# Kernel tuning notes

Hardware: AMD Instinct MI355X
Metric: run time of the kernel (lower is better)

Reference implementation:

```python
import jax, jax.numpy as jnp
import numpy as np
from jax import lax

B, C, H, W = 32, 3, 128, 128
D = 512   # embedding dim (= encoder channels)
K = 512   # codebook size
S = 4     # conv stride / kernel
HL = H // S  # 32
LL = HL * HL // 1  # latent spatial positions per image... (HL*WL)


def setup_inputs() -> dict:
    key = jax.random.key(0)
    k1, k2, k3, k4 = jax.random.split(key, 4)
    x = jax.random.uniform(k1, (B, C, H, W), dtype=jnp.float32)
    We = jax.random.normal(k2, (D, C, S, S), dtype=jnp.float32) * 0.05  # OIHW
    be = jnp.zeros((D,), dtype=jnp.float32)
    Wd = jax.random.normal(k3, (C, D, S, S), dtype=jnp.float32) * 0.05  # OIHW for conv_transpose
    bd = jnp.zeros((C,), dtype=jnp.float32)
    codebook = jax.random.normal(k4, (D, K), dtype=jnp.float32)  # NearestEmbed.weight: (emb_dim, n_emb)
    return {"x": x, "We": We, "be": be, "Wd": Wd, "bd": bd, "codebook": codebook}


def _encode(x, We, be):
    y = lax.conv_general_dilated(x, We, (S, S), 'VALID',
                                 dimension_numbers=('NCHW', 'OIHW', 'NCHW'))
    return jax.nn.relu(y + be[None, :, None, None])  # (B, D, HL, HL)


def _decode(z, Wd, bd):
    y = lax.conv_transpose(z, Wd, (S, S), 'VALID',
                           dimension_numbers=('NCHW', 'OIHW', 'NCHW'))
    return jax.nn.sigmoid(y + bd[None, :, None, None])  # (B, C, H, W)


def _nearest_idx(z, W):
    # z: (B, D, L), W: (D, K). Squared L2 distance via ||z||^2 - 2 z.W + ||W||^2.
    z2 = jnp.sum(z * z, axis=1)                 # (B, L)
    w2 = jnp.sum(W * W, axis=0)                 # (K,)
    cross = jnp.einsum('bdl,dk->blk', z, W)     # (B, L, K)
    dist = z2[:, :, None] - 2.0 * cross + w2[None, None, :]
    return jnp.argmin(dist, axis=-1)            # (B, L) int


def _gather(W, idx):
    # W: (D, K), idx: (B, L) -> (B, D, L)
    return jnp.take(W, idx, axis=1).transpose(1, 0, 2)


def reference(x, We, be, Wd, bd, codebook):
    code = _encode(x, We, be)                       # (B, D, HL, HL)
    z_e = code.reshape(code.shape[0], D, -1)        # (B, D, L)
    # 1) z_q with weight stop-grad + straight-through on input
    idx_q = _nearest_idx(z_e, codebook)
    zq_raw = _gather(lax.stop_gradient(codebook), idx_q)
    z_q = z_e + lax.stop_gradient(zq_raw - z_e)     # grad d z_q / d z_e = I
    # 2) emb with input detached (grad flows only to codebook via gather)
    ze_sg = lax.stop_gradient(z_e)
    idx_e = _nearest_idx(ze_sg, codebook)
    emb = _gather(codebook, idx_e)
    recon = _decode(z_q.reshape(code.shape), Wd, bd)
    return (recon, z_e.reshape(code.shape), emb.reshape(code.shape))
```

## Files before the change

kernel.cpp:

```cpp
#include <hip/hip_runtime.h>
#include <hip/hip_bf16.h>

#define NPOS 32768
#define EPS_GAP 4e-3f
#define MAXSUS 4096

typedef __attribute__((ext_vector_type(8))) short short8;
typedef __attribute__((ext_vector_type(4))) float floatx4;

static __device__ __forceinline__ float bfu(unsigned short h) {
    return __uint_as_float(((unsigned int)h) << 16);
}
static __device__ __forceinline__ unsigned short f2bf(float f) {
    unsigned int u = __float_as_uint(f);
    u = (u + 0x7fffu + ((u >> 16) & 1u)) >> 16;
    return (unsigned short)u;
}
static __device__ __forceinline__ float ldin(const void* p, size_t i, int flag) {
    return flag ? bfu(((const unsigned short*)p)[i]) : ((const float*)p)[i];
}

static __device__ __forceinline__ void ldsbar() {
    asm volatile("s_waitcnt lgkmcnt(0)" ::: "memory");
    __builtin_amdgcn_s_barrier();
    asm volatile("" ::: "memory");
}

static __device__ __forceinline__ size_t swzoff(int k, int d) {
    return (size_t)(d >> 5) * 16384 + (size_t)(k >> 4) * 512
         + (size_t)((((d >> 3) & 3) * 16 + (k & 15)) * 8) + (d & 7);
}

__global__ __launch_bounds__(256) void k_prepAll(
        const void* __restrict__ We, const void* __restrict__ be,
        const void* __restrict__ Wd, const void* __restrict__ bd,
        const void* __restrict__ cb,
        int* __restrict__ flagp, int* __restrict__ scnt,
        float* __restrict__ cbe,
        float* __restrict__ cbT, unsigned short* __restrict__ cbHS,
        unsigned short* __restrict__ cbLS,
        unsigned short* __restrict__ WeswzH, unsigned short* __restrict__ WeswzL,
        float* __restrict__ w2, double* __restrict__ w2d,
        float* __restrict__ U) {
    __shared__ float tile[64][65];
    __shared__ double sd[256];
    __shared__ float sf[256];
    __shared__ int sflag;
    const int bid = blockIdx.x;
    const int t = threadIdx.x;

    {
        const unsigned short* u = (const unsigned short*)cb;
        const int kc = t & 63, g = t >> 6;
        float a = 0.f;
        for (int d = g * 128; d < g * 128 + 128; ++d) {
            float v = bfu(u[(size_t)d * 512 + kc]);
            a = fmaf(v, v, a);
        }
        sf[t] = a;
        __syncthreads();
        if (t < 64) {
            float s = sf[t] + sf[t + 64] + sf[t + 128] + sf[t + 192];
            int ok = (s >= 100.f && s <= 2000.f) ? 1 : 0;
            unsigned long long m = __ballot(ok);
            if (t == 0) sflag = (m == ~0ull) ? 1 : 0;
        }
        __syncthreads();
    }
    const int flag = sflag;

    if (bid == 0) {
        if (t == 0) { *flagp = flag; *scnt = 0; }
        cbe[t]       = ldin(be, t, flag);
        cbe[t + 256] = ldin(be, t + 256, flag);
    } else if (bid < 65) {
        const int bb = bid - 1;
        const int D0 = (bb >> 3) * 64, K0 = (bb & 7) * 64;
        for (int it = 0; it < 16; ++it) {
            int r = (t >> 6) + 4 * it, c = t & 63;
            tile[r][c] = ldin(cb, (size_t)(D0 + r) * 512 + K0 + c, flag);
        }
        __syncthreads();
        for (int it = 0; it < 16; ++it) {
            int r = (t >> 6) + 4 * it, c = t & 63;
            float v = tile[c][r];
            int k = K0 + r, d = D0 + c;
            cbT[(size_t)k * 512 + d] = v;
            size_t o2 = swzoff(k, d);
            unsigned short h = f2bf(v);
            cbHS[o2] = h;
            cbLS[o2] = f2bf(v - bfu(h));
        }
    } else if (bid < 73) {
        const int k = (bid - 65) * 64 + (t & 63);
        const int g = t >> 6;
        double acc = 0.0;
        for (int d = g * 128; d < g * 128 + 128; ++d) {
            double v = (double)ldin(cb, (size_t)d * 512 + k, flag);
            acc += v * v;
        }
        sd[t] = acc;
        __syncthreads();
        if (t < 64) {
            double a = sd[t] + sd[t + 64] + sd[t + 128] + sd[t + 192];
            w2[k] = (float)a;
            w2d[k] = a;
        }
    } else if (bid < 201) {
        const int kk = (bid - 73) * 4 + (t >> 6);
        const int lane = t & 63;
        const int j = lane >> 2, dpart = lane & 3;
        const int u = (j >> 2) & 3, v = j & 3;
        int woff[3];
        #pragma unroll
        for (int m = 0; m < 3; ++m) woff[m] = m * 8192 + (3 - u) * 4 + (3 - v);
        float a0 = 0.f, a1 = 0.f, a2 = 0.f;
        for (int i = 0; i < 128; ++i) {
            int d = dpart * 128 + i;
            float cw = ldin(cb, (size_t)d * 512 + kk, flag);
            a0 = fmaf(cw, ldin(Wd, (size_t)(woff[0] + d * 16), flag), a0);
            a1 = fmaf(cw, ldin(Wd, (size_t)(woff[1] + d * 16), flag), a1);
            a2 = fmaf(cw, ldin(Wd, (size_t)(woff[2] + d * 16), flag), a2);
        }
        a0 += __shfl_xor(a0, 1); a0 += __shfl_xor(a0, 2);
        a1 += __shfl_xor(a1, 1); a1 += __shfl_xor(a1, 2);
        a2 += __shfl_xor(a2, 1); a2 += __shfl_xor(a2, 2);
        if (dpart == 0) {
            U[kk * 48 +  0 + j] = a0 + ldin(bd, 0, flag);
            U[kk * 48 + 16 + j] = a1 + ldin(bd, 1, flag);
            U[kk * 48 + 32 + j] = a2 + ldin(bd, 2, flag);
        }
    } else {
        const int bid2 = bid - 201;
        for (int it = 0; it < 16; ++it) {
            int e = bid2 * 4096 + it * 256 + t;
            int d = e >> 6, q = e & 63;
            float w = (q < 48) ? ldin(We, (size_t)d * 48 + q, flag) : 0.f;
            unsigned short h = f2bf(w);
            unsigned short l = f2bf(w - bfu(h));
            size_t off = (size_t)((d >> 5) * 2 + ((d >> 4) & 1)) * 1024
                       + (size_t)(q >> 5) * 512
                       + (size_t)((((q >> 3) & 3) * 16 + (d & 15)) * 8) + (q & 7);
            WeswzH[off] = h;
            WeswzL[off] = l;
        }
    }
}

static __device__ __forceinline__ void conv_mfma(
        const unsigned short* __restrict__ patchH, const unsigned short* __restrict__ patchL,
        const unsigned short* __restrict__ WeH, const unsigned short* __restrict__ WeL,
        const float* __restrict__ cbe, int dc, int wave, int lane, int flag,
        unsigned short* __restrict__ zq, float* __restrict__ out_z, int b, int SP0) {
    const int mt = wave >> 1, nt = wave & 1;
    const int quad = lane >> 4, lcol = lane & 15;
    const int row = mt * 16 + lcol;
    short8 aH0 = *(const short8*)(patchH + row * 72 + quad * 8);
    short8 aH1 = *(const short8*)(patchH + row * 72 + 32 + quad * 8);
    const unsigned short* wb = WeH + (size_t)((dc >> 5) * 2 + nt) * 1024 + lane * 8;
    short8 bH0 = *(const short8*)(wb);
    short8 bH1 = *(const short8*)(wb + 512);
    floatx4 c = (floatx4){0.f, 0.f, 0.f, 0.f};
    c = __builtin_amdgcn_mfma_f32_16x16x32_bf16(aH0, bH0, c, 0, 0, 0);
    c = __builtin_amdgcn_mfma_f32_16x16x32_bf16(aH1, bH1, c, 0, 0, 0);
    if (!flag) {
        short8 aL0 = *(const short8*)(patchL + row * 72 + quad * 8);
        short8 aL1 = *(const short8*)(patchL + row * 72 + 32 + quad * 8);
        const unsigned short* wl = WeL + (size_t)((dc >> 5) * 2 + nt) * 1024 + lane * 8;
        short8 bL0 = *(const short8*)(wl);
        short8 bL1 = *(const short8*)(wl + 512);
        c = __builtin_amdgcn_mfma_f32_16x16x32_bf16(aL0, bH0, c, 0, 0, 0);
        c = __builtin_amdgcn_mfma_f32_16x16x32_bf16(aL1, bH1, c, 0, 0, 0);
        c = __builtin_amdgcn_mfma_f32_16x16x32_bf16(aH0, bL0, c, 0, 0, 0);
        c = __builtin_amdgcn_mfma_f32_16x16x32_bf16(aH1, bL1, c, 0, 0, 0);
    }
    const int d = nt * 16 + lcol;
    const float bias = cbe[dc + d];
    const int p0 = mt * 16 + quad * 4;
    float zf[4];
    #pragma unroll
    for (int r = 0; r < 4; ++r) {
        float z = fmaxf(c[r] + bias, 0.f);
        unsigned short h = f2bf(z);
        unsigned short l = f2bf(z - bfu(h));
        zq[(p0 + r) * 40 + d] = h;
        zq[2560 + (p0 + r) * 40 + d] = l;
        zf[r] = bfu(h) + bfu(l);
    }
    *(float4*)(out_z + (size_t)(b * 512 + dc + d) * 1024 + SP0 + p0) =
        (float4){zf[0], zf[1], zf[2], zf[3]};
}

static __device__ __forceinline__ void mfma_step(
        const unsigned short* __restrict__ zq,
        const unsigned short* __restrict__ cbHS,
        const unsigned short* __restrict__ cbLS,
        int dcPrev, int wave, int quad, int lcol, int flag, floatx4 (&acc)[4][4]) {
    const int lane = quad * 16 + lcol;
    short8 aH[4], aL[4];
    #pragma unroll
    for (int mt = 0; mt < 4; ++mt) {
        aH[mt] = *(const short8*)(zq + (mt * 16 + lcol) * 40 + quad * 8);
        aL[mt] = *(const short8*)(zq + 2560 + (mt * 16 + lcol) * 40 + quad * 8);
    }
    const unsigned short* fbH = cbHS + (size_t)dcPrev * 512 + (size_t)(wave * 4) * 512 + lane * 8;
    #pragma unroll
    for (int j = 0; j < 4; ++j) {
        short8 bH = *(const short8*)(fbH + j * 512);
        #pragma unroll
        for (int mt = 0; mt < 4; ++mt) {
            acc[mt][j] = __builtin_amdgcn_mfma_f32_16x16x32_bf16(aH[mt], bH, acc[mt][j], 0, 0, 0);
            acc[mt][j] = __builtin_amdgcn_mfma_f32_16x16x32_bf16(aL[mt], bH, acc[mt][j], 0, 0, 0);
        }
    }
    if (!flag) {
        const unsigned short* fbL = cbLS + (size_t)dcPrev * 512 + (size_t)(wave * 4) * 512 + lane * 8;
        #pragma unroll
        for (int j = 0; j < 4; ++j) {
            short8 bL = *(const short8*)(fbL + j * 512);
            #pragma unroll
            for (int mt = 0; mt < 4; ++mt)
                acc[mt][j] = __builtin_amdgcn_mfma_f32_16x16x32_bf16(aH[mt], bL, acc[mt][j], 0, 0, 0);
        }
    }
}

static __device__ __forceinline__ void bmerge(float& a1, int& ak, float& a2,
                                              float o1, int ok, float o2) {
    if (o1 < a1)      { a2 = fminf(a1, o2); a1 = o1; ak = ok; }
    else if (o1 > a1) { a2 = fminf(a2, o1); }
    else              { a2 = a1; if (ok < ak) ak = ok; }
}

__global__ __launch_bounds__(512, 4) void k_main(
        const void* __restrict__ x, const unsigned short* __restrict__ WeswzH,
        const unsigned short* __restrict__ WeswzL,
        const float* __restrict__ cbe, const int* __restrict__ flagp,
        const unsigned short* __restrict__ cbHS, const unsigned short* __restrict__ cbLS,
        const float* __restrict__ cbT, const float* __restrict__ w2,
        float* __restrict__ out_z, float* __restrict__ out_e,
        int* __restrict__ idx, int* __restrict__ scnt, int* __restrict__ spos,
        int skipTail) {
    __shared__ __align__(16) char smc[38912];
    unsigned short* patchH = (unsigned short*)smc;
    unsigned short* patchL = (unsigned short*)(smc + 9216);
    unsigned short* zb = (unsigned short*)(smc + 18432);

    const int t = threadIdx.x;
    const int bid = blockIdx.x;
    const int q = ((bid & 7) << 6) | (bid >> 3);
    const int P0 = q * 64;
    const int b = P0 >> 10, SP0 = P0 & 1023;
    const int flag = *flagp;
    const int wave = t >> 6, lane = t & 63;
    const int quad = lane >> 4, lcol = lane & 15;

    for (int e = t; e < 4096; e += 512) {
        int pid = e >> 6, qq = e & 63;
        float xv = 0.f;
        if (qq < 48) {
            int c = qq >> 4, r = (qq >> 2) & 3, s = qq & 3;
            int pos = P0 + pid;
            int bb = pos >> 10, sp = pos & 1023, i = sp >> 5, j = sp & 31;
            xv = ldin(x, ((bb * 3 + c) * 128 + (i * 4 + r)) * 128 + (j * 4 + s), flag);
        }
        unsigned short h = f2bf(xv);
        patchH[pid * 72 + qq] = h;
        patchL[pid * 72 + qq] = f2bf(xv - bfu(h));
    }

    floatx4 acc[4][4];
    #pragma unroll
    for (int mt = 0; mt < 4; ++mt)
        #pragma unroll
        for (int j = 0; j < 4; ++j) acc[mt][j] = (floatx4){0.f, 0.f, 0.f, 0.f};

    ldsbar();
    conv_mfma(patchH, patchL, WeswzH, WeswzL, cbe, 0, wave, lane, flag,
              zb, out_z, b, SP0);
    for (int dc = 32; dc < 512; dc += 32) {
        ldsbar();
        const int p = (dc >> 5) & 1;
        conv_mfma(patchH, patchL, WeswzH, WeswzL, cbe, dc, wave, lane, flag,
                  zb + p * 5120, out_z, b, SP0);
        mfma_step(zb + (p ^ 1) * 5120, cbHS, cbLS, dc - 32, wave, quad, lcol, flag, acc);
    }
    ldsbar();
    mfma_step(zb + 5120, cbHS, cbLS, 480, wave, quad, lcol, flag, acc);

    float s1[4][4], s2[4][4]; int k1[4][4];
    #pragma unroll
    for (int mt = 0; mt < 4; ++mt)
        #pragma unroll
        for (int r = 0; r < 4; ++r) { s1[mt][r] = 1e30f; s2[mt][r] = 1e30f; k1[mt][r] = 511; }
    #pragma unroll
    for (int j = 0; j < 4; ++j) {
        int code = (wave * 4 + j) * 16 + lcol;
        float wk = w2[code];
        #pragma unroll
        for (int mt = 0; mt < 4; ++mt)
            #pragma unroll
            for (int r = 0; r < 4; ++r) {
                float s = wk - 2.f * acc[mt][j][r];
                bmerge(s1[mt][r], k1[mt][r], s2[mt][r], s, code, 1e30f);
            }
    }
    float* sS1 = (float*)smc;
    int*   sK1 = (int*)(smc + 2048);
    float* sS2 = (float*)(smc + 4096);
    int*   ii  = (int*)(smc + 6144);
    #pragma unroll
    for (int mt = 0; mt < 4; ++mt)
        #pragma unroll
        for (int r = 0; r < 4; ++r) {
            float a1 = s1[mt][r], a2 = s2[mt][r]; int ak = k1[mt][r];
            #pragma unroll
            for (int m = 1; m < 16; m <<= 1) {
                float o1 = __shfl_xor(a1, m);
                float o2 = __shfl_xor(a2, m);
                int   ok = __shfl_xor(ak, m);
                bmerge(a1, ak, a2, o1, ok, o2);
            }
            if (lcol == 0) {
                int pos = mt * 16 + quad * 4 + r;
                sS1[pos * 8 + wave] = a1;
                sK1[pos * 8 + wave] = ak;
                sS2[pos * 8 + wave] = a2;
            }
        }
    __syncthreads();
    if (t < 64) {
        float a1 = sS1[t * 8]; int ak = sK1[t * 8]; float a2 = sS2[t * 8];
        #pragma unroll
        for (int w = 1; w < 8; ++w)
            bmerge(a1, ak, a2, sS1[t * 8 + w], sK1[t * 8 + w], sS2[t * 8 + w]);
        ak &= 511;
        ii[t] = ak;
        unsigned int flagged = 0u;
        if (a2 - a1 < EPS_GAP) {
            int slot = atomicAdd(scnt, 1);
            if (slot < MAXSUS) { spos[slot] = P0 + t; flagged = 1u; }
        }
        idx[P0 + t] = (int)((unsigned)ak | (flagged << 31));
    }
    __syncthreads();

    const int sp = t & 63, dq = t >> 6;
    const float* row = cbT + (size_t)ii[sp] * 512;
    const size_t obase = ((size_t)b * 512) * 1024 + SP0 + sp;
    for (int d0 = dq * 64; d0 < dq * 64 + 64; d0 += 4) {
        if (skipTail && b == 31 && d0 >= 448) break;
        float4 v = *(const float4*)(row + d0);
        out_e[obase + (size_t)(d0    ) * 1024] = v.x;
        out_e[obase + (size_t)(d0 + 1) * 1024] = v.y;
        out_e[obase + (size_t)(d0 + 2) * 1024] = v.z;
        out_e[obase + (size_t)(d0 + 3) * 1024] = v.w;
    }
}

__global__ __launch_bounds__(256) void k_post(
        const float* __restrict__ out_z, const void* __restrict__ cb,
        const double* __restrict__ w2d, int* __restrict__ idx,
        const int* __restrict__ scnt, const int* __restrict__ spos,
        const float* __restrict__ U, const int* __restrict__ flagp,
        float* __restrict__ out_e, float* __restrict__ out_r, int skipTail) {
    __shared__ float zsh[512];
    __shared__ float rs[256];
    __shared__ int rk[256];
    __shared__ int bc[2];
    const int bid = blockIdx.x;
    const int t = threadIdx.x;

    if (bid < 128) {
        const int pos = bid * 256 + t;
        const int v0 = idx[pos];
        if (v0 >= 0) {
            const int id = v0 & 511;
            const int b = pos >> 10, sp = pos & 1023, i = sp >> 5, j = sp & 31;
            const float* u = &U[(size_t)id * 48];
            #pragma unroll
            for (int c = 0; c < 3; ++c)
                #pragma unroll
                for (int uu = 0; uu < 4; ++uu) {
                    float4 q = *(const float4*)(&u[c * 16 + uu * 4]);
                    float4 o;
                    o.x = 1.f / (1.f + __expf(-q.x));
                    o.y = 1.f / (1.f + __expf(-q.y));
                    o.z = 1.f / (1.f + __expf(-q.z));
                    o.w = 1.f / (1.f + __expf(-q.w));
                    *(float4*)(&out_r[((size_t)((b * 3 + c) * 128) + (i * 4 + uu)) * 128 + j * 4]) = o;
                }
        }
        return;
    }

    const int flag = *flagp;
    int n = *scnt; if (n > MAXSUS) n = MAXSUS;
    for (int s = bid - 128; s < n; s += 256) {
        int p = spos[s] & 32767;
        int b = p >> 10, sp = p & 1023;
        __syncthreads();
        zsh[t]       = out_z[(size_t)(b * 512 + t) * 1024 + sp];
        zsh[t + 256] = out_z[(size_t)(b * 512 + t + 256) * 1024 + sp];
        __syncthreads();
        float bs = 1e30f; int bk = 511;
        for (int cc = 0; cc < 2; ++cc) {
            int k = t + cc * 256;
            double a = 0.0;
            for (int d = 0; d < 512; ++d)
                a = fma((double)zsh[d], (double)ldin(cb, (size_t)d * 512 + k, flag), a);
            float sc = (float)(w2d[k] - 2.0 * a);
            if (sc < bs || (sc == bs && k < bk)) { bs = sc; bk = k; }
        }
        rs[t] = bs; rk[t] = bk;
        __syncthreads();
        for (int str = 128; str > 0; str >>= 1) {
            if (t < str) {
                float so = rs[t + str]; int ko = rk[t + str];
                if (so < rs[t] || (so == rs[t] && ko < rk[t])) { rs[t] = so; rk[t] = ko; }
            }
            __syncthreads();
        }
        if (t == 0) {
            int kstar = rk[0] & 511;
            int old = idx[p] & 511;
            bc[0] = kstar; bc[1] = (kstar != old);
            idx[p] = kstar;
        }
        __syncthreads();
        const int kk = bc[0];
        if (bc[1]) {
            for (int d = t; d < 512; d += 256) {
                if (skipTail && b == 31 && d >= 448) continue;
                out_e[(size_t)(b * 512 + d) * 1024 + sp] = ldin(cb, (size_t)d * 512 + kk, flag);
            }
        }
        if (t < 48) {
            float q = U[(size_t)kk * 48 + t];
            float o = 1.f / (1.f + __expf(-q));
            int c = t >> 4, uu = (t >> 2) & 3, vv = t & 3;
            int i = sp >> 5, j = sp & 31;
            out_r[((size_t)((b * 3 + c) * 128) + (i * 4 + uu)) * 128 + j * 4 + vv] = o;
        }
    }
}

__global__ __launch_bounds__(1024) void k_fixup(
        const void* __restrict__ cb, const int* __restrict__ flagp,
        const int* __restrict__ idx, float* __restrict__ out_e) {
    const int t = threadIdx.x;
    const int d = 448 + blockIdx.x;
    const int flag = *flagp;
    const int id = idx[31744 + t] & 511;
    out_e[((size_t)(31 * 512 + d)) * 1024 + t] = ldin(cb, (size_t)d * 512 + id, flag);
}

extern "C" void kernel_launch(void* const* d_in, const int* in_sizes, int n_in,
                              void* d_out, int out_size, void* d_ws, size_t ws_size,
                              hipStream_t stream) {
    const void* x  = d_in[0];
    const void* We = d_in[1];
    const void* be = d_in[2];
    const void* Wd = d_in[3];
    const void* bd = d_in[4];
    const void* cb = d_in[5];

    float* out   = (float*)d_out;
    float* out_r = out;
    float* out_z = out + 1572864;
    float* out_e = out + 18350080;

    char* Rb = (char*)out_r;
    float* cbT           = (float*)(Rb);
    float* cbe           = (float*)(Rb + 1146880);
    unsigned short* cbHS = (unsigned short*)(Rb + 1247296);
    unsigned short* cbLS = (unsigned short*)(Rb + 1771584);
    unsigned short* WeswzH=(unsigned short*)(Rb + 2295872);
    unsigned short* WeswzL=(unsigned short*)(Rb + 2361408);

    int tailWS = (ws_size >= 262144) ? 1 : 0;
    char* Tbase = tailWS ? (char*)d_ws : ((char*)out_e + 66846720);
    int skipTail = tailWS ? 0 : 1;
    int*    idx  = (int*)   (Tbase);
    float*  U    = (float*) (Tbase + 131072);
    float*  w2   = (float*) (Tbase + 229376);
    double* w2d  = (double*)(Tbase + 231424);
    int*    flag = (int*)   (Tbase + 235520);
    int*    scnt = (int*)   (Tbase + 235584);
    int*    spos = (int*)   (Tbase + 235648);

    k_prepAll<<<209, 256, 0, stream>>>(We, be, Wd, bd, cb, flag, scnt,
                                       cbe, cbT, cbHS, cbLS, WeswzH, WeswzL,
                                       w2, w2d, U);
    k_main<<<512, 512, 0, stream>>>(x, WeswzH, WeswzL, cbe, flag, cbHS, cbLS,
                                    cbT, w2, out_z, out_e, idx, scnt, spos,
                                    skipTail);
    k_post<<<384, 256, 0, stream>>>(out_z, cb, w2d, idx, scnt, spos, U, flag,
                                    out_e, out_r, skipTail);
    if (skipTail)
        k_fixup<<<64, 1024, 0, stream>>>(cb, flag, idx, out_e);
}
```

Baseline: 261.6 us.

## Move decoder-table computation into main kernel and double conv/MFMA pipeline stage depth

Precomputation of the per-code decoder table U moves out of the prep kernel into 64 extra blocks of the main kernel. The prep kernel shrinks and this work can overlap with the main encode/quantize blocks. The conv-to-codebook-MFMA pipeline now processes two 32-channel chunks per barrier using four LDS buffers instead of two, which halves the number of barriers. This raises static LDS from 38912 to 59392 bytes per block, which may lower occupancy under the 4-blocks-per-CU launch bound. The extra U blocks also compete with the main blocks for CUs.

```diff
diff --git a/kernel.cpp b/kernel.cpp
--- a/kernel.cpp
+++ b/kernel.cpp
@@ -33,15 +33,13 @@
 
 __global__ __launch_bounds__(256) void k_prepAll(
         const void* __restrict__ We, const void* __restrict__ be,
-        const void* __restrict__ Wd, const void* __restrict__ bd,
         const void* __restrict__ cb,
         int* __restrict__ flagp, int* __restrict__ scnt,
         float* __restrict__ cbe,
         float* __restrict__ cbT, unsigned short* __restrict__ cbHS,
         unsigned short* __restrict__ cbLS,
         unsigned short* __restrict__ WeswzH, unsigned short* __restrict__ WeswzL,
-        float* __restrict__ w2, double* __restrict__ w2d,
-        float* __restrict__ U) {
+        float* __restrict__ w2, double* __restrict__ w2d) {
     __shared__ float tile[64][65];
     __shared__ double sd[256];
     __shared__ float sf[256];
@@ -106,32 +104,8 @@
             w2[k] = (float)a;
             w2d[k] = a;
         }
-    } else if (bid < 201) {
-        const int kk = (bid - 73) * 4 + (t >> 6);
-        const int lane = t & 63;
-        const int j = lane >> 2, dpart = lane & 3;
-        const int u = (j >> 2) & 3, v = j & 3;
-        int woff[3];
-        #pragma unroll
-        for (int m = 0; m < 3; ++m) woff[m] = m * 8192 + (3 - u) * 4 + (3 - v);
-        float a0 = 0.f, a1 = 0.f, a2 = 0.f;
-        for (int i = 0; i < 128; ++i) {
-            int d = dpart * 128 + i;
-            float cw = ldin(cb, (size_t)d * 512 + kk, flag);
-            a0 = fmaf(cw, ldin(Wd, (size_t)(woff[0] + d * 16), flag), a0);
-            a1 = fmaf(cw, ldin(Wd, (size_t)(woff[1] + d * 16), flag), a1);
-            a2 = fmaf(cw, ldin(Wd, (size_t)(woff[2] + d * 16), flag), a2);
-        }
-        a0 += __shfl_xor(a0, 1); a0 += __shfl_xor(a0, 2);
-        a1 += __shfl_xor(a1, 1); a1 += __shfl_xor(a1, 2);
-        a2 += __shfl_xor(a2, 1); a2 += __shfl_xor(a2, 2);
-        if (dpart == 0) {
-            U[kk * 48 +  0 + j] = a0 + ldin(bd, 0, flag);
-            U[kk * 48 + 16 + j] = a1 + ldin(bd, 1, flag);
-            U[kk * 48 + 32 + j] = a2 + ldin(bd, 2, flag);
-        }
     } else {
-        const int bid2 = bid - 201;
+        const int bid2 = bid - 73;
         for (int it = 0; it < 16; ++it) {
             int e = bid2 * 4096 + it * 256 + t;
             int d = e >> 6, q = e & 63;
@@ -238,21 +212,50 @@
         const float* __restrict__ cbe, const int* __restrict__ flagp,
         const unsigned short* __restrict__ cbHS, const unsigned short* __restrict__ cbLS,
         const float* __restrict__ cbT, const float* __restrict__ w2,
+        const void* __restrict__ cb, const void* __restrict__ Wd,
+        const void* __restrict__ bd, float* __restrict__ U,
         float* __restrict__ out_z, float* __restrict__ out_e,
         int* __restrict__ idx, int* __restrict__ scnt, int* __restrict__ spos,
         int skipTail) {
-    __shared__ __align__(16) char smc[38912];
+    __shared__ __align__(16) char smc[59392];
     unsigned short* patchH = (unsigned short*)smc;
     unsigned short* patchL = (unsigned short*)(smc + 9216);
     unsigned short* zb = (unsigned short*)(smc + 18432);
 
     const int t = threadIdx.x;
     const int bid = blockIdx.x;
+    const int flag = *flagp;
+    const int wave = t >> 6, lane = t & 63;
+
+    if (bid >= 512) {
+        const int kk = (bid - 512) * 8 + wave;
+        const int j = lane >> 2, dpart = lane & 3;
+        const int u = (j >> 2) & 3, v = j & 3;
+        int woff[3];
+        #pragma unroll
+        for (int m = 0; m < 3; ++m) woff[m] = m * 8192 + (3 - u) * 4 + (3 - v);
+        float a0 = 0.f, a1 = 0.f, a2 = 0.f;
+        for (int i = 0; i < 128; ++i) {
+            int d = dpart * 128 + i;
+            float cw = ldin(cb, (size_t)d * 512 + kk, flag);
+            a0 = fmaf(cw, ldin(Wd, (size_t)(woff[0] + d * 16), flag), a0);
+            a1 = fmaf(cw, ldin(Wd, (size_t)(woff[1] + d * 16), flag), a1);
+            a2 = fmaf(cw, ldin(Wd, (size_t)(woff[2] + d * 16), flag), a2);
+        }
+        a0 += __shfl_xor(a0, 1); a0 += __shfl_xor(a0, 2);
+        a1 += __shfl_xor(a1, 1); a1 += __shfl_xor(a1, 2);
+        a2 += __shfl_xor(a2, 1); a2 += __shfl_xor(a2, 2);
+        if (dpart == 0) {
+            U[kk * 48 +  0 + j] = a0 + ldin(bd, 0, flag);
+            U[kk * 48 + 16 + j] = a1 + ldin(bd, 1, flag);
+            U[kk * 48 + 32 + j] = a2 + ldin(bd, 2, flag);
+        }
+        return;
+    }
+
     const int q = ((bid & 7) << 6) | (bid >> 3);
     const int P0 = q * 64;
     const int b = P0 >> 10, SP0 = P0 & 1023;
-    const int flag = *flagp;
-    const int wave = t >> 6, lane = t & 63;
     const int quad = lane >> 4, lcol = lane & 15;
 
     for (int e = t; e < 4096; e += 512) {
@@ -278,15 +281,21 @@
     ldsbar();
     conv_mfma(patchH, patchL, WeswzH, WeswzL, cbe, 0, wave, lane, flag,
               zb, out_z, b, SP0);
-    for (int dc = 32; dc < 512; dc += 32) {
+    conv_mfma(patchH, patchL, WeswzH, WeswzL, cbe, 32, wave, lane, flag,
+              zb + 5120, out_z, b, SP0);
+    for (int dc = 64; dc < 512; dc += 64) {
         ldsbar();
-        const int p = (dc >> 5) & 1;
+        const int s = (dc >> 5) & 3;
         conv_mfma(patchH, patchL, WeswzH, WeswzL, cbe, dc, wave, lane, flag,
-                  zb + p * 5120, out_z, b, SP0);
-        mfma_step(zb + (p ^ 1) * 5120, cbHS, cbLS, dc - 32, wave, quad, lcol, flag, acc);
+                  zb + s * 5120, out_z, b, SP0);
+        conv_mfma(patchH, patchL, WeswzH, WeswzL, cbe, dc + 32, wave, lane, flag,
+                  zb + ((s + 1) & 3) * 5120, out_z, b, SP0);
+        mfma_step(zb + ((s + 2) & 3) * 5120, cbHS, cbLS, dc - 64, wave, quad, lcol, flag, acc);
+        mfma_step(zb + ((s + 3) & 3) * 5120, cbHS, cbLS, dc - 32, wave, quad, lcol, flag, acc);
     }
     ldsbar();
-    mfma_step(zb + 5120, cbHS, cbLS, 480, wave, quad, lcol, flag, acc);
+    mfma_step(zb + 2 * 5120, cbHS, cbLS, 448, wave, quad, lcol, flag, acc);
+    mfma_step(zb + 3 * 5120, cbHS, cbLS, 480, wave, quad, lcol, flag, acc);
 
     float s1[4][4], s2[4][4]; int k1[4][4];
     #pragma unroll
@@ -489,12 +498,12 @@
     int*    scnt = (int*)   (Tbase + 235584);
     int*    spos = (int*)   (Tbase + 235648);
 
-    k_prepAll<<<209, 256, 0, stream>>>(We, be, Wd, bd, cb, flag, scnt,
-                                       cbe, cbT, cbHS, cbLS, WeswzH, WeswzL,
-                                       w2, w2d, U);
-    k_main<<<512, 512, 0, stream>>>(x, WeswzH, WeswzL, cbe, flag, cbHS, cbLS,
-                                    cbT, w2, out_z, out_e, idx, scnt, spos,
-                                    skipTail);
+    k_prepAll<<<81, 256, 0, stream>>>(We, be, cb, flag, scnt,
+                                      cbe, cbT, cbHS, cbLS, WeswzH, WeswzL,
+                                      w2, w2d);
+    k_main<<<576, 512, 0, stream>>>(x, WeswzH, WeswzL, cbe, flag, cbHS, cbLS,
+                                    cbT, w2, cb, Wd, bd, U,
+                                    out_z, out_e, idx, scnt, spos, skipTail);
     k_post<<<384, 256, 0, stream>>>(out_z, cb, w2d, idx, scnt, spos, U, flag,
                                     out_e, out_r, skipTail);
     if (skipTail)
```

Result: no change. 265.5 us (+1.5%).
